# Kernel tuning notes

Measured on AMD Instinct MI355X. Metric: run time of the kernel, lower is better.

The kernel has to match this reference:

```python
import jax, jax.numpy as jnp
import numpy as np

N_OSC = 50
N_PER = 40
DT = 0.01
STEPS = 100
# one-link torque limb physical constants (reconstructed)
M_G_LC = 1.0   # m*g*lc gravity torque coefficient
B_DAMP = 0.1   # viscous damping
I_INERTIA = 1.0


def setup_inputs() -> dict:
    key = jax.random.key(0)
    ks = jax.random.split(key, 16)
    B = 8192
    x = jax.random.normal(ks[0], (B, 2), dtype=jnp.float32)
    fc1_w = jax.random.normal(ks[1], (128, 2), dtype=jnp.float32) * 0.5
    fc1_b = jax.random.normal(ks[2], (128,), dtype=jnp.float32) * 0.1
    fc2_w = jax.random.normal(ks[3], (128, 128), dtype=jnp.float32) * 0.08
    fc2_b = jax.random.normal(ks[4], (128,), dtype=jnp.float32) * 0.1
    fc3_w = jax.random.normal(ks[5], (N_OSC * 2, 128), dtype=jnp.float32) * 0.08
    fc3_b = jax.random.normal(ks[6], (N_OSC * 2,), dtype=jnp.float32) * 0.1
    fcd_w = jax.random.normal(ks[7], (1, 128), dtype=jnp.float32) * 0.001  # weight/100
    fcd_b = jnp.zeros((1,), dtype=jnp.float32)                            # bias*0
    enc = jax.random.normal(ks[8], (N_OSC, N_PER, 2), dtype=jnp.float32)
    obias = jax.random.normal(ks[9], (N_OSC, N_PER), dtype=jnp.float32)
    dec = jax.random.normal(ks[10], (N_OSC, 2, N_PER), dtype=jnp.float32) * 0.05
    fc4_w = jax.random.normal(ks[11], (1, N_OSC * N_PER), dtype=jnp.float32) * 1e-4  # weight/10000
    fc4_b = jnp.zeros((1,), dtype=jnp.float32)                                       # bias*0
    return {"x": x, "fc1_w": fc1_w, "fc1_b": fc1_b, "fc2_w": fc2_w, "fc2_b": fc2_b,
            "fc3_w": fc3_w, "fc3_b": fc3_b, "fcd_w": fcd_w, "fcd_b": fcd_b,
            "enc": enc, "obias": obias, "dec": dec, "fc4_w": fc4_w, "fc4_b": fc4_b}


def reference(x, fc1_w, fc1_b, fc2_w, fc2_b, fc3_w, fc3_b, fcd_w, fcd_b,
              enc, obias, dec, fc4_w, fc4_b):
    B = x.shape[0]
    h = jax.nn.relu(x @ fc1_w.T + fc1_b)            # (B,128)
    direct = h @ fcd_w.T + fcd_b                    # (B,1)
    h2 = jax.nn.relu(h @ fc2_w.T + fc2_b)           # (B,128)
    x3 = h2 @ fc3_w.T + fc3_b                       # (B, 2*N_OSC)
    o0 = x3.reshape(B, N_OSC, 2).transpose(1, 0, 2)  # (N_OSC,B,2), xi = x[:, 2j:2j+2]
    l0 = jnp.concatenate([x[:, :1], jnp.zeros((B, 1), dtype=x.dtype)], axis=1)  # (B,2)

    def step(carry, _):
        o, l = carry
        # NEF oscillator activities: relu(state @ encoders^T + bias), vectorized over oscillators
        a = jax.nn.relu(jnp.einsum('obd,ond->obn', o, enc) + obias[:, None, :])  # (N_OSC,B,N_PER)
        o_deriv = jnp.einsum('odn,obn->obd', dec, a)                             # (N_OSC,B,2)
        o = o + DT * o_deriv
        acts = a.transpose(1, 0, 2).reshape(B, N_OSC * N_PER)                    # (B,2000)
        torque = (acts @ fc4_w.T + fc4_b + direct)[:, 0]                         # (B,)
        theta, omega = l[:, 0], l[:, 1]
        alpha = (torque - M_G_LC * jnp.sin(theta) - B_DAMP * omega) / I_INERTIA
        l = l + DT * jnp.stack([omega, alpha], axis=1)
        return (o, l), (l, torque)

    _, (l_states, torques) = jax.lax.scan(step, (o0, l0), None, length=STEPS)
    return l_states, torques  # (STEPS,B,2), (STEPS,B)
```

## Files before the change

kernel.cpp:

```cpp
#include <hip/hip_runtime.h>

#define N_OSC 50
#define N_PER 40
#define DT 0.01f
#define STEPS 100
#define BATCH 8192

typedef float v2f __attribute__((ext_vector_type(2)));

static __device__ __forceinline__ v2f fma2(v2f a, v2f b, v2f c) {
    return __builtin_elementwise_fma(a, b, c);
}

#define WS_PC     0
#define WS_DIRECT 12288
#define WS_O0     20480
#define WS_TORQ   839680

__global__ __launch_bounds__(256) void prep_kernel(
    const float* __restrict__ enc, const float* __restrict__ obias,
    const float* __restrict__ dec, const float* __restrict__ fc4_w,
    float* __restrict__ pc, float* __restrict__ torq) {
    int idx = blockIdx.x * 256 + threadIdx.x;
    ((float4*)torq)[idx] = make_float4(0.f, 0.f, 0.f, 0.f);
    if (idx < N_OSC * N_PER) {
        int o = idx / N_PER, n = idx - o * N_PER;
        int i = n >> 1, h = n & 1;
        float* base = pc + o * 240;
        base[4 * i + h]           = enc[o * 80 + 2 * n + 0];
        base[4 * i + 2 + h]       = enc[o * 80 + 2 * n + 1];
        base[80 + 4 * i + h]      = dec[o * 80 + n];
        base[80 + 4 * i + 2 + h]  = dec[o * 80 + 40 + n];
        base[160 + 2 * i + h]     = fc4_w[o * 40 + n];
        base[200 + n]             = obias[o * 40 + n];
    }
}

__global__ __launch_bounds__(256) void mlp_kernel(
    const float* __restrict__ x,
    const float* __restrict__ fc1_w, const float* __restrict__ fc1_b,
    const float* __restrict__ fc2_w, const float* __restrict__ fc2_b,
    const float* __restrict__ fc3_w, const float* __restrict__ fc3_b,
    const float* __restrict__ fcd_w, const float* __restrict__ fcd_b,
    float* __restrict__ o0out, float* __restrict__ directout) {
    __shared__ float hs[32 * 132];
    __shared__ float h2s[32 * 132];
    int tid = threadIdx.x;
    int bb = tid & 31;
    int hw = tid >> 5;
    int b0 = blockIdx.x * 32;

    for (int idx = tid; idx < 32 * 128; idx += 256) {
        int r = idx >> 7, j = idx & 127;
        float x0 = x[(b0 + r) * 2], x1 = x[(b0 + r) * 2 + 1];
        float v = fmaf(x0, fc1_w[j * 2], fmaf(x1, fc1_w[j * 2 + 1], fc1_b[j]));
        hs[r * 132 + j] = fmaxf(v, 0.f);
    }
    __syncthreads();

    if (tid < 32) {
        float s = fcd_b[0];
        #pragma unroll 8
        for (int k = 0; k < 128; k += 4) {
            float4 h4 = *(const float4*)&hs[tid * 132 + k];
            float4 w4 = *(const float4*)&fcd_w[k];
            s = fmaf(h4.x, w4.x, fmaf(h4.y, w4.y, fmaf(h4.z, w4.z, fmaf(h4.w, w4.w, s))));
        }
        directout[b0 + tid] = s;
    }

    for (int pass = 0; pass < 4; ++pass) {
        int j0 = hw * 16 + pass * 4;
        float a0 = fc2_b[j0], a1 = fc2_b[j0 + 1], a2 = fc2_b[j0 + 2], a3 = fc2_b[j0 + 3];
        const float* w0 = fc2_w + j0 * 128;
        const float* w1 = w0 + 128;
        const float* w2 = w0 + 256;
        const float* w3 = w0 + 384;
        #pragma unroll 8
        for (int k = 0; k < 128; k += 4) {
            float4 h4 = *(const float4*)&hs[bb * 132 + k];
            float4 q0 = *(const float4*)&w0[k];
            float4 q1 = *(const float4*)&w1[k];
            float4 q2 = *(const float4*)&w2[k];
            float4 q3 = *(const float4*)&w3[k];
            a0 = fmaf(h4.x, q0.x, fmaf(h4.y, q0.y, fmaf(h4.z, q0.z, fmaf(h4.w, q0.w, a0))));
            a1 = fmaf(h4.x, q1.x, fmaf(h4.y, q1.y, fmaf(h4.z, q1.z, fmaf(h4.w, q1.w, a1))));
            a2 = fmaf(h4.x, q2.x, fmaf(h4.y, q2.y, fmaf(h4.z, q2.z, fmaf(h4.w, q2.w, a2))));
            a3 = fmaf(h4.x, q3.x, fmaf(h4.y, q3.y, fmaf(h4.z, q3.z, fmaf(h4.w, q3.w, a3))));
        }
        h2s[bb * 132 + j0]     = fmaxf(a0, 0.f);
        h2s[bb * 132 + j0 + 1] = fmaxf(a1, 0.f);
        h2s[bb * 132 + j0 + 2] = fmaxf(a2, 0.f);
        h2s[bb * 132 + j0 + 3] = fmaxf(a3, 0.f);
    }
    __syncthreads();

    for (int pass = 0; pass < 4; ++pass) {
        int j0 = pass * 32 + hw * 4;
        if (j0 >= 100) continue;
        float a0 = fc3_b[j0], a1 = fc3_b[j0 + 1], a2 = fc3_b[j0 + 2], a3 = fc3_b[j0 + 3];
        const float* w0 = fc3_w + j0 * 128;
        const float* w1 = w0 + 128;
        const float* w2 = w0 + 256;
        const float* w3 = w0 + 384;
        #pragma unroll 8
        for (int k = 0; k < 128; k += 4) {
            float4 h4 = *(const float4*)&h2s[bb * 132 + k];
            float4 q0 = *(const float4*)&w0[k];
            float4 q1 = *(const float4*)&w1[k];
            float4 q2 = *(const float4*)&w2[k];
            float4 q3 = *(const float4*)&w3[k];
            a0 = fmaf(h4.x, q0.x, fmaf(h4.y, q0.y, fmaf(h4.z, q0.z, fmaf(h4.w, q0.w, a0))));
            a1 = fmaf(h4.x, q1.x, fmaf(h4.y, q1.y, fmaf(h4.z, q1.z, fmaf(h4.w, q1.w, a1))));
            a2 = fmaf(h4.x, q2.x, fmaf(h4.y, q2.y, fmaf(h4.z, q2.z, fmaf(h4.w, q2.w, a2))));
            a3 = fmaf(h4.x, q3.x, fmaf(h4.y, q3.y, fmaf(h4.z, q3.z, fmaf(h4.w, q3.w, a3))));
        }
        o0out[(j0)     * BATCH + b0 + bb] = a0;
        o0out[(j0 + 1) * BATCH + b0 + bb] = a1;
        o0out[(j0 + 2) * BATCH + b0 + bb] = a2;
        o0out[(j0 + 3) * BATCH + b0 + bb] = a3;
    }
}

__global__ __launch_bounds__(64, 2) void osc_kernel(const float* __restrict__ pc,
                                                    const float* __restrict__ o0init,
                                                    float* __restrict__ torq) {
    __shared__ float cs[240];
    int blk = blockIdx.x;
    int bg = blk / N_OSC;
    int osc = blk - bg * N_OSC;
    int tid = threadIdx.x;
    int b = bg * 64 + tid;

    if (tid < 60)
        ((float4*)cs)[tid] = ((const float4*)(pc + osc * 240))[tid];
    __syncthreads();

    v2f e0[20], e1[20], d0c[20], d1c[20], wc[20];
    #pragma unroll
    for (int i = 0; i < 20; ++i) {
        e0[i]  = *(const v2f*)(cs + 4 * i);
        e1[i]  = *(const v2f*)(cs + 4 * i + 2);
        d0c[i] = *(const v2f*)(cs + 80 + 4 * i);
        d1c[i] = *(const v2f*)(cs + 80 + 4 * i + 2);
        wc[i]  = *(const v2f*)(cs + 160 + 2 * i);
    }
    #pragma unroll
    for (int i = 0; i < 20; ++i) {
        asm volatile("" : "+v"(e0[i]));
        asm volatile("" : "+v"(e1[i]));
        asm volatile("" : "+v"(d0c[i]));
        asm volatile("" : "+v"(d1c[i]));
        asm volatile("" : "+v"(wc[i]));
    }

    float ob[40];
    #pragma unroll
    for (int n = 0; n < 40; ++n) {
        union { float f; int i; } u;
        u.f = cs[200 + n];
        u.i = __builtin_amdgcn_readfirstlane(u.i);
        ob[n] = u.f;
    }

    float s0 = o0init[(2 * osc) * BATCH + b];
    float s1 = o0init[(2 * osc + 1) * BATCH + b];

    for (int step = 0; step < STEPS; ++step) {
        v2f o0p = (v2f){s0, s0};
        v2f o1p = (v2f){s1, s1};
        v2f tq = (v2f){0.f, 0.f};
        v2f D0 = (v2f){0.f, 0.f};
        v2f D1 = (v2f){0.f, 0.f};
        #pragma unroll
        for (int i = 0; i < 20; ++i) {
            v2f obp = (v2f){ob[2 * i], ob[2 * i + 1]};
            v2f a = fma2(o0p, e0[i], fma2(o1p, e1[i], obp));
            a = __builtin_elementwise_max(a, (v2f){0.f, 0.f});
            tq = fma2(a, wc[i], tq);
            D0 = fma2(a, d0c[i], D0);
            D1 = fma2(a, d1c[i], D1);
        }
        s0 = fmaf(DT, D0.x + D0.y, s0);
        s1 = fmaf(DT, D1.x + D1.y, s1);
        atomicAdd(&torq[step * BATCH + b], tq.x + tq.y);
    }
}

__global__ __launch_bounds__(256) void pend_kernel(const float* __restrict__ x,
                                                   const float* __restrict__ torq,
                                                   const float* __restrict__ direct,
                                                   const float* __restrict__ fc4_b,
                                                   float* __restrict__ out) {
    int b = blockIdx.x * 256 + threadIdx.x;
    float theta = x[2 * b];
    float omega = 0.f;
    float base = direct[b] + fc4_b[0];
    float2* out_l = (float2*)out;
    float* out_t = out + STEPS * BATCH * 2;
    float pf[4];
    #pragma unroll
    for (int j = 0; j < 4; ++j) pf[j] = torq[j * BATCH + b];
    #pragma unroll 4
    for (int s = 0; s < STEPS; ++s) {
        float tq = base + pf[s & 3];
        if (s + 4 < STEPS) pf[s & 3] = torq[(s + 4) * BATCH + b];
        float alpha = tq - __sinf(theta) - 0.1f * omega;
        theta = fmaf(DT, omega, theta);
        omega = fmaf(DT, alpha, omega);
        out_l[s * BATCH + b] = make_float2(theta, omega);
        out_t[s * BATCH + b] = tq;
    }
}

extern "C" void kernel_launch(void* const* d_in, const int* in_sizes, int n_in,
                              void* d_out, int out_size, void* d_ws, size_t ws_size,
                              hipStream_t stream) {
    const float* x     = (const float*)d_in[0];
    const float* fc1_w = (const float*)d_in[1];
    const float* fc1_b = (const float*)d_in[2];
    const float* fc2_w = (const float*)d_in[3];
    const float* fc2_b = (const float*)d_in[4];
    const float* fc3_w = (const float*)d_in[5];
    const float* fc3_b = (const float*)d_in[6];
    const float* fcd_w = (const float*)d_in[7];
    const float* fcd_b = (const float*)d_in[8];
    const float* enc   = (const float*)d_in[9];
    const float* obias = (const float*)d_in[10];
    const float* dec   = (const float*)d_in[11];
    const float* fc4_w = (const float*)d_in[12];
    const float* fc4_b = (const float*)d_in[13];
    float* out = (float*)d_out;
    float* ws = (float*)d_ws;

    float* pc      = ws + WS_PC;
    float* direct  = ws + WS_DIRECT;
    float* o0      = ws + WS_O0;
    float* torq    = ws + WS_TORQ;

    hipLaunchKernelGGL(prep_kernel, dim3(STEPS * BATCH / 4 / 256), dim3(256), 0, stream,
                       enc, obias, dec, fc4_w, pc, torq);
    hipLaunchKernelGGL(mlp_kernel, dim3(256), dim3(256), 0, stream,
                       x, fc1_w, fc1_b, fc2_w, fc2_b, fc3_w, fc3_b,
                       fcd_w, fcd_b, o0, direct);
    hipLaunchKernelGGL(osc_kernel, dim3(128 * N_OSC), dim3(64), 0, stream,
                       pc, o0, torq);
    hipLaunchKernelGGL(pend_kernel, dim3(BATCH / 256), dim3(256), 0, stream,
                       x, torq, direct, fc4_b, out);
}
```

Before: 414.2 us.

## Split oscillator neurons across four waves with shared-memory reduction; fuse prep into MLP

The oscillator kernel now uses 256-thread blocks where each of four waves handles 10 of the 40 neurons for the same 64 batch elements. Partial derivative and torque sums are exchanged through double-buffered shared memory with a barrier every step, and one wave does the torque atomic. This cuts per-thread register use and the serial inner loop, raising parallelism, at the cost of a per-step __syncthreads and LDS traffic. The prep and MLP kernels are merged into one launch, and the pendulum kernel uses 64-thread blocks to spread across more CUs.

```diff
diff --git a/kernel.cpp b/kernel.cpp
--- a/kernel.cpp
+++ b/kernel.cpp
@@ -17,38 +17,41 @@
 #define WS_O0     20480
 #define WS_TORQ   839680
 
-__global__ __launch_bounds__(256) void prep_kernel(
-    const float* __restrict__ enc, const float* __restrict__ obias,
-    const float* __restrict__ dec, const float* __restrict__ fc4_w,
-    float* __restrict__ pc, float* __restrict__ torq) {
-    int idx = blockIdx.x * 256 + threadIdx.x;
-    ((float4*)torq)[idx] = make_float4(0.f, 0.f, 0.f, 0.f);
-    if (idx < N_OSC * N_PER) {
-        int o = idx / N_PER, n = idx - o * N_PER;
-        int i = n >> 1, h = n & 1;
-        float* base = pc + o * 240;
-        base[4 * i + h]           = enc[o * 80 + 2 * n + 0];
-        base[4 * i + 2 + h]       = enc[o * 80 + 2 * n + 1];
-        base[80 + 4 * i + h]      = dec[o * 80 + n];
-        base[80 + 4 * i + 2 + h]  = dec[o * 80 + 40 + n];
-        base[160 + 2 * i + h]     = fc4_w[o * 40 + n];
-        base[200 + n]             = obias[o * 40 + n];
-    }
-}
-
-__global__ __launch_bounds__(256) void mlp_kernel(
+__global__ __launch_bounds__(256) void prep_mlp_kernel(
     const float* __restrict__ x,
     const float* __restrict__ fc1_w, const float* __restrict__ fc1_b,
     const float* __restrict__ fc2_w, const float* __restrict__ fc2_b,
     const float* __restrict__ fc3_w, const float* __restrict__ fc3_b,
     const float* __restrict__ fcd_w, const float* __restrict__ fcd_b,
+    const float* __restrict__ enc, const float* __restrict__ obias,
+    const float* __restrict__ dec, const float* __restrict__ fc4_w,
+    float* __restrict__ pc, float* __restrict__ torq,
     float* __restrict__ o0out, float* __restrict__ directout) {
     __shared__ float hs[32 * 132];
     __shared__ float h2s[32 * 132];
+    int blk = blockIdx.x;
     int tid = threadIdx.x;
+
+    if (blk < 800) {
+        int idx = blk * 256 + tid;
+        ((float4*)torq)[idx] = make_float4(0.f, 0.f, 0.f, 0.f);
+        if (idx < N_OSC * N_PER) {
+            int o = idx / N_PER, n = idx - o * N_PER;
+            int c = n >> 1, h = n & 1;
+            float* base = pc + o * 240;
+            base[4 * c + h]           = enc[o * 80 + 2 * n + 0];
+            base[4 * c + 2 + h]       = enc[o * 80 + 2 * n + 1];
+            base[80 + 4 * c + h]      = dec[o * 80 + n];
+            base[80 + 4 * c + 2 + h]  = dec[o * 80 + 40 + n];
+            base[160 + 2 * c + h]     = fc4_w[o * 40 + n];
+            base[200 + n]             = obias[o * 40 + n];
+        }
+        return;
+    }
+
     int bb = tid & 31;
     int hw = tid >> 5;
-    int b0 = blockIdx.x * 32;
+    int b0 = (blk - 800) * 32;
 
     for (int idx = tid; idx < 32 * 128; idx += 256) {
         int r = idx >> 7, j = idx & 127;
@@ -122,45 +125,34 @@
     }
 }
 
-__global__ __launch_bounds__(64, 2) void osc_kernel(const float* __restrict__ pc,
-                                                    const float* __restrict__ o0init,
-                                                    float* __restrict__ torq) {
+__global__ __launch_bounds__(256, 4) void osc_kernel(const float* __restrict__ pc,
+                                                     const float* __restrict__ o0init,
+                                                     float* __restrict__ torq) {
     __shared__ float cs[240];
+    __shared__ float4 xch[2][256];
     int blk = blockIdx.x;
     int bg = blk / N_OSC;
     int osc = blk - bg * N_OSC;
     int tid = threadIdx.x;
-    int b = bg * 64 + tid;
+    int lane = tid & 63;
+    int w = tid >> 6;
+    int b = bg * 64 + lane;
 
     if (tid < 60)
         ((float4*)cs)[tid] = ((const float4*)(pc + osc * 240))[tid];
     __syncthreads();
 
-    v2f e0[20], e1[20], d0c[20], d1c[20], wc[20];
+    v2f e0[5], e1[5], d0c[5], d1c[5], wcv[5], obv[5];
+    int c0 = w * 5;
     #pragma unroll
-    for (int i = 0; i < 20; ++i) {
-        e0[i]  = *(const v2f*)(cs + 4 * i);
-        e1[i]  = *(const v2f*)(cs + 4 * i + 2);
-        d0c[i] = *(const v2f*)(cs + 80 + 4 * i);
-        d1c[i] = *(const v2f*)(cs + 80 + 4 * i + 2);
-        wc[i]  = *(const v2f*)(cs + 160 + 2 * i);
-    }
-    #pragma unroll
-    for (int i = 0; i < 20; ++i) {
-        asm volatile("" : "+v"(e0[i]));
-        asm volatile("" : "+v"(e1[i]));
-        asm volatile("" : "+v"(d0c[i]));
-        asm volatile("" : "+v"(d1c[i]));
-        asm volatile("" : "+v"(wc[i]));
-    }
-
-    float ob[40];
-    #pragma unroll
-    for (int n = 0; n < 40; ++n) {
-        union { float f; int i; } u;
-        u.f = cs[200 + n];
-        u.i = __builtin_amdgcn_readfirstlane(u.i);
-        ob[n] = u.f;
+    for (int i = 0; i < 5; ++i) {
+        int c = c0 + i;
+        e0[i]  = *(const v2f*)(cs + 4 * c);
+        e1[i]  = *(const v2f*)(cs + 4 * c + 2);
+        d0c[i] = *(const v2f*)(cs + 80 + 4 * c);
+        d1c[i] = *(const v2f*)(cs + 80 + 4 * c + 2);
+        wcv[i] = *(const v2f*)(cs + 160 + 2 * c);
+        obv[i] = *(const v2f*)(cs + 200 + 2 * c);
     }
 
     float s0 = o0init[(2 * osc) * BATCH + b];
@@ -173,26 +165,37 @@
         v2f D0 = (v2f){0.f, 0.f};
         v2f D1 = (v2f){0.f, 0.f};
         #pragma unroll
-        for (int i = 0; i < 20; ++i) {
-            v2f obp = (v2f){ob[2 * i], ob[2 * i + 1]};
-            v2f a = fma2(o0p, e0[i], fma2(o1p, e1[i], obp));
+        for (int i = 0; i < 5; ++i) {
+            v2f a = fma2(o0p, e0[i], fma2(o1p, e1[i], obv[i]));
             a = __builtin_elementwise_max(a, (v2f){0.f, 0.f});
-            tq = fma2(a, wc[i], tq);
+            tq = fma2(a, wcv[i], tq);
             D0 = fma2(a, d0c[i], D0);
             D1 = fma2(a, d1c[i], D1);
         }
-        s0 = fmaf(DT, D0.x + D0.y, s0);
-        s1 = fmaf(DT, D1.x + D1.y, s1);
-        atomicAdd(&torq[step * BATCH + b], tq.x + tq.y);
-    }
-}
-
-__global__ __launch_bounds__(256) void pend_kernel(const float* __restrict__ x,
-                                                   const float* __restrict__ torq,
-                                                   const float* __restrict__ direct,
-                                                   const float* __restrict__ fc4_b,
-                                                   float* __restrict__ out) {
-    int b = blockIdx.x * 256 + threadIdx.x;
+        int p = step & 1;
+        xch[p][tid] = make_float4(D0.x + D0.y, D1.x + D1.y, tq.x + tq.y, 0.f);
+        __syncthreads();
+        float4 q0 = xch[p][lane];
+        float4 q1 = xch[p][64 + lane];
+        float4 q2 = xch[p][128 + lane];
+        float4 q3 = xch[p][192 + lane];
+        float dd0 = (q0.x + q1.x) + (q2.x + q3.x);
+        float dd1 = (q0.y + q1.y) + (q2.y + q3.y);
+        s0 = fmaf(DT, dd0, s0);
+        s1 = fmaf(DT, dd1, s1);
+        if (w == 0) {
+            float tt = (q0.z + q1.z) + (q2.z + q3.z);
+            atomicAdd(&torq[step * BATCH + b], tt);
+        }
+    }
+}
+
+__global__ __launch_bounds__(64) void pend_kernel(const float* __restrict__ x,
+                                                  const float* __restrict__ torq,
+                                                  const float* __restrict__ direct,
+                                                  const float* __restrict__ fc4_b,
+                                                  float* __restrict__ out) {
+    int b = blockIdx.x * 64 + threadIdx.x;
     float theta = x[2 * b];
     float omega = 0.f;
     float base = direct[b] + fc4_b[0];
@@ -238,13 +241,12 @@
     float* o0      = ws + WS_O0;
     float* torq    = ws + WS_TORQ;
 
-    hipLaunchKernelGGL(prep_kernel, dim3(STEPS * BATCH / 4 / 256), dim3(256), 0, stream,
-                       enc, obias, dec, fc4_w, pc, torq);
-    hipLaunchKernelGGL(mlp_kernel, dim3(256), dim3(256), 0, stream,
+    hipLaunchKernelGGL(prep_mlp_kernel, dim3(800 + 256), dim3(256), 0, stream,
                        x, fc1_w, fc1_b, fc2_w, fc2_b, fc3_w, fc3_b,
-                       fcd_w, fcd_b, o0, direct);
-    hipLaunchKernelGGL(osc_kernel, dim3(128 * N_OSC), dim3(64), 0, stream,
+                       fcd_w, fcd_b, enc, obias, dec, fc4_w,
+                       pc, torq, o0, direct);
+    hipLaunchKernelGGL(osc_kernel, dim3(128 * N_OSC), dim3(256), 0, stream,
                        pc, o0, torq);
-    hipLaunchKernelGGL(pend_kernel, dim3(BATCH / 256), dim3(256), 0, stream,
+    hipLaunchKernelGGL(pend_kernel, dim3(BATCH / 64), dim3(64), 0, stream,
                        x, torq, direct, fc4_b, out);
 }
```

New measurement: 473.8 us. +14.4%, slower.
